# Kernel optimization log

Hardware: AMD Instinct MI355X
Metric: run time of the kernel (lower is better)

Reference implementation:

```python
import jax, jax.numpy as jnp
import numpy as np

B = 1024; PAST = 64; FUT = 16; N = PAST + FUT; DM = N // 3; HID = 64
EMB = [(2000, 32), (7, 8), (24, 8)]
OUTP = 3 + 32 + 8 + 8  # 51 = out_preprocess
O = OUTP - 1           # 50
HID1 = 64; HID2 = 64
NEG = -1e30  # finite stand-in for -inf so fully-masked rows stay NaN-free


def _gcnn(x, A, W, act):
    # D = diag((1 + rowsum(sign(relu(A-1e-15))))^-0.5); out = act(D @ A @ D @ (x W^T))
    d = (1.0 + (A > 1e-15).astype(x.dtype).sum(1)) ** -0.5
    An = d[:, None] * A * d[None, :]            # (P,P)
    h = jnp.einsum('pq,bqc->bpc', An, x @ W.T)  # (B,P,out)
    return jax.nn.relu(h) if act else h


def _forward(data, emb0, emb1, emb2, w1, b1, w2, b2, w3, b3,
             M, Wg1a, Wg1b, Wk, smoothing, Wg2a, Wg2b):
    # learned adjacency: masked softmax over strictly-lower-triangular support
    mask = jnp.tril(jnp.ones((N, N), data.dtype), -1)
    A0 = jax.nn.relu(M @ M.T)
    A = jax.nn.softmax(jnp.where(mask > 0, A0, NEG), axis=1)
    A = jnp.where(mask > 0, A, 0.0)
    # pre_processing: embeddings + MLP, then re-append last raw column
    tabs = (emb0, emb1, emb2)
    e = [t[data[:, :, i].astype(jnp.int32)] for i, t in enumerate(tabs)]
    h = jnp.concatenate(e + [data[:, :, -3:]], -1)        # (B,N,51)
    h = jax.nn.relu(h @ w1.T + b1)
    h = jax.nn.relu(h @ w2.T + b2)
    h = h @ w3.T + b3                                      # (B,N,50)
    x = jnp.concatenate([h, data[:, :, -1:]], -1)          # (B,N,51)
    sg1, sg2 = x[:, :PAST], x[:, PAST:]
    A11 = A[:PAST, :PAST]
    x1 = _gcnn(_gcnn(sg1, A11, Wg1a, True), A11, Wg1b, False)   # (B,PAST,50)
    xk = jnp.concatenate([x1, sg2[:, :, :-1]], 1)               # (B,N,50)
    y = x[:, :PAST, -1:]                                        # (B,PAST,1)
    # Kernel: batched Mahalanobis quadratic form (diagonal computed directly)
    xp, xf = xk[:, :PAST], xk[:, PAST:]
    theta = Wk @ Wk.T
    theta = (theta + theta.T) / 2
    diff = xp[:, None, :, :] - xf[:, :, None, :]                # (B,F,P,50)
    q = jnp.einsum('bjip,pq,bjiq->bji', diff, theta, diff)      # (B,F,P)
    alpha = -0.5 * q / (jax.nn.sigmoid(smoothing[0]) * 0.01)
    At = A[FUT:, :PAST] if False else A[PAST:, :PAST]           # (F,P)
    At = jax.nn.softmax(jnp.where(At != 0, At, NEG), axis=1)
    # torch Softmax(dim=1) on (B,F,P) normalizes over the F axis
    alpha = jax.nn.softmax(jnp.where(At[None] >= 0.004, alpha, NEG), axis=1)
    yh = jnp.einsum('bjp,bpo->bjo', alpha, y)                   # (B,F,1)
    x2 = jnp.concatenate([sg2[:, :, :-1], yh], -1)              # (B,F,51)
    A22 = A[PAST:, PAST:]
    out = _gcnn(_gcnn(x2, A22, Wg2a, True), A22, Wg2b, False).reshape(-1, FUT)
    # cdist(x, x), p=2, with NaN-safe sqrt at zero distance
    xc = jnp.concatenate([sg1, x2], 1)                          # (B,N,51)
    sq = jnp.sum(xc * xc, -1)
    d2 = jnp.maximum(sq[:, :, None] + sq[:, None, :]
                     - 2.0 * jnp.einsum('bnc,bmc->bnm', xc, xc), 0.0)
    dist = jnp.where(d2 > 0, jnp.sqrt(jnp.where(d2 > 0, d2, 1.0)), 0.0)
    return (out, dist, A)


def setup_inputs() -> dict:
    key = jax.random.key(0)
    ks = jax.random.split(key, 20)
    cols = [jax.random.randint(ks[i], (B, N, 1), 0, EMB[i][0]).astype(jnp.float32)
            for i in range(3)]
    data = jnp.concatenate(cols + [jax.random.normal(ks[3], (B, N, 3), jnp.float32)], -1)
    g = lambda k, s, sc: jax.random.normal(k, s, jnp.float32) * sc
    return dict(
        data=data,
        emb0=g(ks[4], EMB[0], 1.0),
        emb1=g(ks[5], EMB[1], 1.0),
        emb2=g(ks[6], EMB[2], 1.0),
        w1=g(ks[7], (128, OUTP), OUTP ** -0.5), b1=jnp.zeros((128,), jnp.float32),
        w2=g(ks[8], (128, 128), 128 ** -0.5), b2=jnp.zeros((128,), jnp.float32),
        w3=g(ks[9], (O, 128), 128 ** -0.5), b3=jnp.zeros((O,), jnp.float32),
        M=g(ks[10], (N, DM), 1.0),
        Wg1a=g(ks[11], (HID1, OUTP), OUTP ** -0.5),
        Wg1b=g(ks[12], (O, HID1), HID1 ** -0.5),
        Wk=g(ks[13], (O, HID), 0.05),
        smoothing=g(ks[14], (1,), 1.0),
        Wg2a=g(ks[15], (HID2, OUTP), OUTP ** -0.5),
        Wg2b=g(ks[16], (1, HID2), HID2 ** -0.5),
    )


def reference(data, emb0, emb1, emb2, w1, b1, w2, b2, w3, b3,
              M, Wg1a, Wg1b, Wk, smoothing, Wg2a, Wg2b):
    return _forward(data, emb0, emb1, emb2, w1, b1, w2, b2, w3, b3,
                    M, Wg1a, Wg1b, Wk, smoothing, Wg2a, Wg2b)
```

## Files before the change

kernel.cpp:

```cpp
#include <hip/hip_runtime.h>
#include <math.h>


#define NEGBIG (-1e30f)

#define OFF_X     0
#define OFF_A     7471104
#define OFF_AN22  7481600
#define OFF_MK    7484356
#define OFF_GAH   7514692
#define OFF_GAL   7516740
#define OFF_G2AT  7521156
#define OFF_SC    7524420
#define OFF_W1H   7524424
#define OFF_W1L   7528520
#define OFF_W2H   7532616
#define OFF_W2L   7540808
#define OFF_W3H   7549000
#define OFF_W3L   7553096
#define OFF_ANH   7557192
#define OFF_ANL   7559240
#define OFF_GBH   7561288
#define OFF_GBL   7563336
#define OFF_WKH   7565384
#define OFF_WKL   7567432

#define OUT_OUT   0
#define OUT_DIST  16384
#define OUT_A     6569984

typedef __attribute__((ext_vector_type(8))) short bf16x8;
typedef __attribute__((ext_vector_type(4))) short s16x4;
typedef __attribute__((ext_vector_type(4))) float f32x4;

__device__ __forceinline__ unsigned short f2bf(float x) {
  union { float f; unsigned u; } v; v.f = x;
  unsigned r = v.u + 0x7fffu + ((v.u >> 16) & 1u);
  return (unsigned short)(r >> 16);
}
__device__ __forceinline__ float bf2f(unsigned short h) {
  union { unsigned u; float f; } v; v.u = ((unsigned)h) << 16; return v.f;
}
__device__ __forceinline__ void split2(float v, unsigned short& h, unsigned short& l) {
  unsigned short hh = f2bf(v);
  h = hh;
  l = f2bf(v - bf2f(hh));
}
#define SWZ6(r, k) (((r) << 6) + (((((k) >> 3) ^ ((r) & 7)) << 3) | ((k) & 7)))
#define SWZ7(r, k) (((r) << 7) + (((((k) >> 3) ^ ((r) & 7)) << 3) | ((k) & 7)))

#define MFMA3(acc, aH, aL, bH, bL) \
  acc = __builtin_amdgcn_mfma_f32_16x16x32_bf16(aH, bH, acc, 0, 0, 0); \
  acc = __builtin_amdgcn_mfma_f32_16x16x32_bf16(aH, bL, acc, 0, 0, 0); \
  acc = __builtin_amdgcn_mfma_f32_16x16x32_bf16(aL, bH, acc, 0, 0, 0);
#define MFMA4(acc, aH, aL, bH, bL) \
  MFMA3(acc, aH, aL, bH, bL) \
  acc = __builtin_amdgcn_mfma_f32_16x16x32_bf16(aL, bL, acc, 0, 0, 0);

__global__ __launch_bounds__(256) void k_prep(
    const float* __restrict__ M, const float* __restrict__ Wk,
    const float* __restrict__ sm,
    const float* __restrict__ w1, const float* __restrict__ w2,
    const float* __restrict__ w3,
    const float* __restrict__ wg1a, const float* __restrict__ wg1b,
    const float* __restrict__ wg2a,
    float* __restrict__ ws, float* __restrict__ out)
{
  __shared__ float Msh[80 * 26];
  __shared__ float Ash[80 * 80];
  __shared__ float d1[64];
  __shared__ float d2s[16];
  const int t = threadIdx.x;

  if (blockIdx.x == 0) {
    for (int e = t; e < 80 * 26; e += 256) Msh[e] = M[e];
    __syncthreads();
    for (int e = t; e < 6400; e += 256) {
      int i = e / 80, j = e % 80;
      float v = 0.f;
      if (j < i) {
        float s = 0.f;
        for (int k = 0; k < 26; ++k) s += Msh[i * 26 + k] * Msh[j * 26 + k];
        v = s > 0.f ? s : 0.f;
      }
      Ash[e] = v;
    }
    __syncthreads();
    if (t > 0 && t < 80) {
      int i = t;
      float m = -3.4e38f;
      for (int j = 0; j < i; ++j) m = fmaxf(m, Ash[i * 80 + j]);
      float s = 0.f;
      for (int j = 0; j < i; ++j) {
        float e = expf(Ash[i * 80 + j] - m);
        Ash[i * 80 + j] = e;
        s += e;
      }
      float inv = 1.f / s;
      for (int j = 0; j < i; ++j) Ash[i * 80 + j] *= inv;
    }
    __syncthreads();
    {
      float* Aws = ws + OFF_A;
      float* Aout = out + OUT_A;
      for (int e = t; e < 6400; e += 256) { Aws[e] = Ash[e]; Aout[e] = Ash[e]; }
    }
    if (t < 64) {
      int c = 0;
      for (int j = 0; j < 64; ++j) if (Ash[t * 80 + j] > 1e-15f) ++c;
      d1[t] = 1.f / sqrtf(1.f + (float)c);
    } else if (t < 80) {
      int i = t - 64; int c = 0;
      for (int j = 0; j < 16; ++j) if (Ash[(64 + i) * 80 + 64 + j] > 1e-15f) ++c;
      d2s[i] = 1.f / sqrtf(1.f + (float)c);
    }
    __syncthreads();
    {
      float* an22 = ws + OFF_AN22;
      unsigned short* anH = (unsigned short*)(ws + OFF_ANH);
      unsigned short* anL = (unsigned short*)(ws + OFF_ANL);
      for (int e = t; e < 4096; e += 256) {
        int i = e >> 6, j = e & 63;
        float v = d1[i] * Ash[i * 80 + j] * d1[j];
        unsigned short h = f2bf(v);
        anH[e] = h; anL[e] = f2bf(v - bf2f(h));
      }
      for (int e = t; e < 256; e += 256) {
        int i = e >> 4, j = e & 15;
        an22[e] = d2s[i] * Ash[(64 + i) * 80 + 64 + j] * d2s[j];
      }
    }
    if (t < 16) {
      float* mk = ws + OFF_MK;
      int j = t;
      float m = -3.4e38f;
      for (int i = 0; i < 64; ++i) {
        float v = Ash[(64 + j) * 80 + i];
        v = (v != 0.f) ? v : NEGBIG;
        m = fmaxf(m, v);
      }
      float s = 0.f;
      for (int i = 0; i < 64; ++i) {
        float v = Ash[(64 + j) * 80 + i];
        v = (v != 0.f) ? v : NEGBIG;
        s += expf(v - m);
      }
      float inv = 1.f / s;
      for (int i = 0; i < 64; ++i) {
        float v = Ash[(64 + j) * 80 + i];
        v = (v != 0.f) ? v : NEGBIG;
        mk[j * 64 + i] = (expf(v - m) * inv >= 0.004f) ? 1.f : 0.f;
      }
    }
  } else if (blockIdx.x == 1) {
    unsigned short* wkh = (unsigned short*)(ws + OFF_WKH);
    unsigned short* wkl = (unsigned short*)(ws + OFF_WKL);
    for (int e = t; e < 4096; e += 256) {
      int h = e >> 6, o = e & 63;
      float v = (o < 50) ? Wk[o * 64 + h] : 0.f;
      unsigned short hh = f2bf(v);
      wkh[e] = hh; wkl[e] = f2bf(v - bf2f(hh));
    }
    if (t == 0) {
      float v = sm[0];
      float sig = 1.f / (1.f + expf(-v));
      (ws + OFF_SC)[0] = -0.5f / (sig * 0.01f);
    }
  } else if (blockIdx.x == 2) {
    unsigned short* w1h = (unsigned short*)(ws + OFF_W1H);
    unsigned short* w1l = (unsigned short*)(ws + OFF_W1L);
    for (int e = t; e < 8192; e += 256) {
      int n = e >> 6, k = e & 63;
      float v = (k < 51) ? w1[n * 51 + k] : 0.f;
      unsigned short h = f2bf(v);
      w1h[e] = h; w1l[e] = f2bf(v - bf2f(h));
    }
    unsigned short* w3h = (unsigned short*)(ws + OFF_W3H);
    unsigned short* w3l = (unsigned short*)(ws + OFF_W3L);
    for (int e = t; e < 8192; e += 256) {
      int n = e >> 7, k = e & 127;
      float v = (n < 50) ? w3[n * 128 + k] : 0.f;
      unsigned short h = f2bf(v);
      w3h[e] = h; w3l[e] = f2bf(v - bf2f(h));
    }
    unsigned short* gah = (unsigned short*)(ws + OFF_GAH);
    unsigned short* gal = (unsigned short*)(ws + OFF_GAL);
    for (int e = t; e < 4096; e += 256) {
      int n = e >> 6, k = e & 63;
      float v = (k < 51) ? wg1a[n * 51 + k] : 0.f;
      unsigned short h = f2bf(v);
      gah[e] = h; gal[e] = f2bf(v - bf2f(h));
    }
  } else {
    unsigned short* w2h = (unsigned short*)(ws + OFF_W2H);
    unsigned short* w2l = (unsigned short*)(ws + OFF_W2L);
    for (int e = t; e < 16384; e += 256) {
      int n = e >> 7, k = e & 127;
      float v = w2[n * 128 + k];
      unsigned short h = f2bf(v);
      w2h[e] = h; w2l[e] = f2bf(v - bf2f(h));
    }
    unsigned short* gbh = (unsigned short*)(ws + OFF_GBH);
    unsigned short* gbl = (unsigned short*)(ws + OFF_GBL);
    for (int e = t; e < 4096; e += 256) {
      int n = e >> 6, k = e & 63;
      float v = (n < 50) ? wg1b[n * 64 + k] : 0.f;
      unsigned short h = f2bf(v);
      gbh[e] = h; gbl[e] = f2bf(v - bf2f(h));
    }
    float* g2at = ws + OFF_G2AT;
    for (int e = t; e < 64 * 51; e += 256) { int o = e / 51, k = e % 51; g2at[k * 64 + o] = wg2a[e]; }
  }
}

__global__ __launch_bounds__(512) void k_mlp(
    const float* __restrict__ data,
    const float* __restrict__ emb0, const float* __restrict__ emb1,
    const float* __restrict__ emb2,
    const float* __restrict__ b1, const float* __restrict__ b2,
    const float* __restrict__ b3,
    float* __restrict__ ws)
{
  __shared__ __align__(16) unsigned short actH[64 * 128];
  __shared__ __align__(16) unsigned short actL[64 * 128];
  __shared__ __align__(16) unsigned short wbH[8192];
  __shared__ __align__(16) unsigned short wbL[8192];
  const int t = threadIdx.x;
  const int lane = t & 63, wave = t >> 6;
  const int s = wave & 3, half = wave >> 2;
  const int m16 = lane & 15, quad = lane >> 4;
  const int base = blockIdx.x * 64;
  const int row0 = s * 16;
  const int arow = row0 + m16;
  const unsigned short* w1h = (const unsigned short*)(ws + OFF_W1H);
  const unsigned short* w1l = (const unsigned short*)(ws + OFF_W1L);
  const unsigned short* w2h = (const unsigned short*)(ws + OFF_W2H);
  const unsigned short* w2l = (const unsigned short*)(ws + OFF_W2L);
  const unsigned short* w3h = (const unsigned short*)(ws + OFF_W3H);
  const unsigned short* w3l = (const unsigned short*)(ws + OFF_W3L);
  float* x = ws + OFF_X;

  for (int e = t; e < 4096; e += 512) {
    int r = e >> 6, c = e & 63;
    int g = base + r;
    float v = 0.f;
    if (c < 32)      { int i0 = (int)data[g * 6 + 0]; v = emb0[i0 * 32 + c]; }
    else if (c < 40) { int i1 = (int)data[g * 6 + 1]; v = emb1[i1 * 8 + (c - 32)]; }
    else if (c < 48) { int i2 = (int)data[g * 6 + 2]; v = emb2[i2 * 8 + (c - 40)]; }
    else if (c < 51) { v = data[g * 6 + 3 + (c - 48)]; }
    int idx = SWZ7(r, c);
    split2(v, actH[idx], actL[idx]);
  }
  for (int q = t; q < 1024; q += 512) {
    int col = q >> 3, c = q & 7;
    int dst = (col << 6) + ((c ^ (col & 7)) << 3);
    *(bf16x8*)(wbH + dst) = *(const bf16x8*)(w1h + (col << 6) + (c << 3));
    *(bf16x8*)(wbL + dst) = *(const bf16x8*)(w1l + (col << 6) + (c << 3));
  }
  bf16x8 pH[2], pL[2];
#pragma unroll
  for (int i = 0; i < 2; ++i) {
    int q = t + i * 512;
    int coll = q >> 4, c = q & 15;
    int src = (coll << 7) + (c << 3);
    pH[i] = *(const bf16x8*)(w2h + src);
    pL[i] = *(const bf16x8*)(w2l + src);
  }
  if (t < 64) x[(base + t) * 51 + 50] = data[(base + t) * 6 + 5];
  __syncthreads();

  {
    f32x4 acc[4];
#pragma unroll
    for (int n = 0; n < 4; ++n) acc[n] = (f32x4){0.f, 0.f, 0.f, 0.f};
#pragma unroll
    for (int kb8 = 0; kb8 < 8; kb8 += 4) {
      int ach = ((quad + kb8) ^ (m16 & 7)) << 3;
      bf16x8 aH = *(const bf16x8*)(actH + (arow << 7) + ach);
      bf16x8 aL = *(const bf16x8*)(actL + (arow << 7) + ach);
#pragma unroll
      for (int n = 0; n < 4; ++n) {
        const int col = (half * 4 + n) * 16 + m16;
        int boff = (col << 6) + ach;
        bf16x8 bH = *(const bf16x8*)(wbH + boff);
        bf16x8 bL = *(const bf16x8*)(wbL + boff);
        MFMA3(acc[n], aH, aL, bH, bL)
      }
    }
#pragma unroll
    for (int n = 0; n < 4; ++n) {
      const int col = (half * 4 + n) * 16 + m16;
      const float bias = b1[col];
#pragma unroll
      for (int r = 0; r < 4; ++r) {
        float v = acc[n][r] + bias; v = v > 0.f ? v : 0.f;
        int idx = SWZ7(row0 + quad * 4 + r, col);
        split2(v, actH[idx], actL[idx]);
      }
    }
  }
  __syncthreads();

#pragma unroll
  for (int i = 0; i < 2; ++i) {
    int q = t + i * 512;
    int coll = q >> 4, c = q & 15;
    int dst = (coll << 7) + ((c ^ (coll & 7)) << 3);
    *(bf16x8*)(wbH + dst) = pH[i];
    *(bf16x8*)(wbL + dst) = pL[i];
  }
#pragma unroll
  for (int i = 0; i < 2; ++i) {
    int q = t + i * 512;
    int coll = q >> 4, c = q & 15;
    int src = ((64 + coll) << 7) + (c << 3);
    pH[i] = *(const bf16x8*)(w2h + src);
    pL[i] = *(const bf16x8*)(w2l + src);
  }
  __syncthreads();

  f32x4 acc2[2][2];
#pragma unroll
  for (int a2 = 0; a2 < 2; ++a2)
#pragma unroll
    for (int n = 0; n < 2; ++n) acc2[a2][n] = (f32x4){0.f, 0.f, 0.f, 0.f};
#pragma unroll
  for (int kb8 = 0; kb8 < 16; kb8 += 4) {
    int ach = ((quad + kb8) ^ (m16 & 7)) << 3;
    bf16x8 aH = *(const bf16x8*)(actH + (arow << 7) + ach);
    bf16x8 aL = *(const bf16x8*)(actL + (arow << 7) + ach);
#pragma unroll
    for (int n = 0; n < 2; ++n) {
      const int cl = (half * 2 + n) * 16 + m16;
      int boff = (cl << 7) + ach;
      bf16x8 bH = *(const bf16x8*)(wbH + boff);
      bf16x8 bL = *(const bf16x8*)(wbL + boff);
      MFMA3(acc2[0][n], aH, aL, bH, bL)
    }
  }
  __syncthreads();

#pragma unroll
  for (int i = 0; i < 2; ++i) {
    int q = t + i * 512;
    int coll = q >> 4, c = q & 15;
    int dst = (coll << 7) + ((c ^ (coll & 7)) << 3);
    *(bf16x8*)(wbH + dst) = pH[i];
    *(bf16x8*)(wbL + dst) = pL[i];
  }
#pragma unroll
  for (int i = 0; i < 2; ++i) {
    int q = t + i * 512;
    int coll = q >> 4, c = q & 15;
    int src = (coll << 7) + (c << 3);
    pH[i] = *(const bf16x8*)(w3h + src);
    pL[i] = *(const bf16x8*)(w3l + src);
  }
  __syncthreads();

#pragma unroll
  for (int kb8 = 0; kb8 < 16; kb8 += 4) {
    int ach = ((quad + kb8) ^ (m16 & 7)) << 3;
    bf16x8 aH = *(const bf16x8*)(actH + (arow << 7) + ach);
    bf16x8 aL = *(const bf16x8*)(actL + (arow << 7) + ach);
#pragma unroll
    for (int n = 0; n < 2; ++n) {
      const int cl = (half * 2 + n) * 16 + m16;
      int boff = (cl << 7) + ach;
      bf16x8 bH = *(const bf16x8*)(wbH + boff);
      bf16x8 bL = *(const bf16x8*)(wbL + boff);
      MFMA3(acc2[1][n], aH, aL, bH, bL)
    }
  }
  __syncthreads();

#pragma unroll
  for (int hh = 0; hh < 2; ++hh) {
#pragma unroll
    for (int n = 0; n < 2; ++n) {
      const int col = hh * 64 + (half * 2 + n) * 16 + m16;
      const float bias = b2[col];
#pragma unroll
      for (int r = 0; r < 4; ++r) {
        float v = acc2[hh][n][r] + bias; v = v > 0.f ? v : 0.f;
        int idx = SWZ7(row0 + quad * 4 + r, col);
        split2(v, actH[idx], actL[idx]);
      }
    }
  }
#pragma unroll
  for (int i = 0; i < 2; ++i) {
    int q = t + i * 512;
    int coll = q >> 4, c = q & 15;
    int dst = (coll << 7) + ((c ^ (coll & 7)) << 3);
    *(bf16x8*)(wbH + dst) = pH[i];
    *(bf16x8*)(wbL + dst) = pL[i];
  }
  __syncthreads();

  {
    f32x4 acc[2];
#pragma unroll
    for (int n = 0; n < 2; ++n) acc[n] = (f32x4){0.f, 0.f, 0.f, 0.f};
#pragma unroll
    for (int kb8 = 0; kb8 < 16; kb8 += 4) {
      int ach = ((quad + kb8) ^ (m16 & 7)) << 3;
      bf16x8 aH = *(const bf16x8*)(actH + (arow << 7) + ach);
      bf16x8 aL = *(const bf16x8*)(actL + (arow << 7) + ach);
#pragma unroll
      for (int n = 0; n < 2; ++n) {
        const int col = (half * 2 + n) * 16 + m16;
        int boff = (col << 7) + ach;
        bf16x8 bH = *(const bf16x8*)(wbH + boff);
        bf16x8 bL = *(const bf16x8*)(wbL + boff);
        MFMA3(acc[n], aH, aL, bH, bL)
      }
    }
#pragma unroll
    for (int n = 0; n < 2; ++n) {
      const int col = (half * 2 + n) * 16 + m16;
      if (col < 50) {
        const float bias = b3[col];
#pragma unroll
        for (int r = 0; r < 4; ++r) {
          int row = row0 + quad * 4 + r;
          x[(base + row) * 51 + col] = acc[n][r] + bias;
        }
      }
    }
  }
}

__global__ __launch_bounds__(512) void k_gqd(const float* __restrict__ wg2b,
                                             float* __restrict__ ws,
                                             float* __restrict__ out)
{
  __shared__ __align__(16) unsigned short SH[32768];
  unsigned short* b1H = SH;
  unsigned short* b1L = SH + 4096;
  unsigned short* b2H = SH + 8192;
  unsigned short* b2L = SH + 12288;
  unsigned short* anH = SH + 16384;
  unsigned short* anL = SH + 20480;
  unsigned short* wH  = SH + 24576;
  unsigned short* wL  = SH + 28672;
  unsigned short* xfH = SH + 24576;
  unsigned short* xfL = SH + 25600;
  unsigned short* zfH = SH + 26624;
  unsigned short* zfL = SH + 27648;
  float* alS  = (float*)(SH + 28672);
  float* spH2 = (float*)(SH + 30848);
  float* spS  = (float*)(SH + 31104);
  float* sfS  = (float*)(SH + 31232);
  float* yvS  = (float*)(SH + 31264);
  float* yhsS = (float*)(SH + 31392);
  float* X2v  = (float*)(SH + 8192);
  float* A22v = X2v + 832;
  float* G2v  = A22v + 256;
  float* Pmv  = G2v + 1024;
  float* wb2  = Pmv + 1024;
  float* zzv  = wb2 + 64;
  unsigned short* xcH = SH;
  unsigned short* xcL = SH + 16384;
  float* sqS = (float*)(SH + 21504);

  const int t = threadIdx.x, b = blockIdx.x;
  const int lane = t & 63, wave = t >> 6;
  const int s = wave & 3, half = wave >> 2;
  const int m16 = lane & 15, quad = lane >> 4;
  const int row0 = s * 16;
  const int arow = row0 + m16;
  const float* x = ws + OFF_X;
  const float* mk = ws + OFF_MK;
  const float* an22 = ws + OFF_AN22;
  const float* g2at = ws + OFF_G2AT;
  const unsigned short* gAnH = (const unsigned short*)(ws + OFF_ANH);
  const unsigned short* gAnL = (const unsigned short*)(ws + OFF_ANL);
  const unsigned short* gaH = (const unsigned short*)(ws + OFF_GAH);
  const unsigned short* gaL = (const unsigned short*)(ws + OFF_GAL);
  const unsigned short* gbH = (const unsigned short*)(ws + OFF_GBH);
  const unsigned short* gbL = (const unsigned short*)(ws + OFF_GBL);
  const unsigned short* gwkH = (const unsigned short*)(ws + OFF_WKH);
  const unsigned short* gwkL = (const unsigned short*)(ws + OFF_WKL);
  const float sc = (ws + OFF_SC)[0];

  for (int e = t; e < 4096; e += 512) {
    int r = e >> 6, k = e & 63;
    float v = (k < 51) ? x[(b * 80 + r) * 51 + k] : 0.f;
    int idx = SWZ6(r, k);
    split2(v, b1H[idx], b1L[idx]);
  }
  {
    int q = t;
    if (q < 512) {
      int r = q >> 3, c = q & 7;
      int dst = (r << 6) + ((c ^ (r & 7)) << 3);
      int src = (r << 6) + (c << 3);
      *(bf16x8*)(anH + dst) = *(const bf16x8*)(gAnH + src);
      *(bf16x8*)(anL + dst) = *(const bf16x8*)(gAnL + src);
      *(bf16x8*)(wH + dst)  = *(const bf16x8*)(gaH + src);
      *(bf16x8*)(wL + dst)  = *(const bf16x8*)(gaL + src);
    }
  }
  float yvreg = 0.f;
  if (t < 64) yvreg = x[(b * 80 + t) * 51 + 50];
  bf16x8 pH, pL;
  {
    int q = t & 511;
    int r = q >> 3, c = q & 7;
    int src = (r << 6) + (c << 3);
    pH = *(const bf16x8*)(gbH + src);
    pL = *(const bf16x8*)(gbL + src);
  }
  __syncthreads();

  f32x4 accA[2];
#pragma unroll
  for (int n = 0; n < 2; ++n) accA[n] = (f32x4){0.f, 0.f, 0.f, 0.f};
#pragma unroll
  for (int kb8 = 0; kb8 < 8; kb8 += 4) {
    int ach = ((quad + kb8) ^ (m16 & 7)) << 3;
    bf16x8 aH = *(const bf16x8*)(b1H + (arow << 6) + ach);
    bf16x8 aL = *(const bf16x8*)(b1L + (arow << 6) + ach);
#pragma unroll
    for (int n = 0; n < 2; ++n) {
      const int col = (half * 2 + n) * 16 + m16;
      int boff = (col << 6) + ach;
      bf16x8 bH = *(const bf16x8*)(wH + boff);
      bf16x8 bL = *(const bf16x8*)(wL + boff);
      MFMA3(accA[n], aH, aL, bH, bL)
    }
  }
  __syncthreads();

  {
    const int kb = row0 + quad * 4;
#pragma unroll
    for (int n = 0; n < 2; ++n) {
      const int col = (half * 2 + n) * 16 + m16;
      int idx = (col << 6) + (((((kb >> 3) ^ (col & 7)) << 3)) | (kb & 7));
      s16x4 hv, lv;
#pragma unroll
      for (int r = 0; r < 4; ++r) {
        unsigned short hh, ll; split2(accA[n][r], hh, ll);
        hv[r] = (short)hh; lv[r] = (short)ll;
      }
      *(s16x4*)(b2H + idx) = hv; *(s16x4*)(b2L + idx) = lv;
    }
  }
  {
    int q = t & 511;
    int r = q >> 3, c = q & 7;
    int dst = (r << 6) + ((c ^ (r & 7)) << 3);
    *(bf16x8*)(wH + dst) = pH;
    *(bf16x8*)(wL + dst) = pL;
    int src = (r << 6) + (c << 3);
    pH = *(const bf16x8*)(gwkH + src);
    pL = *(const bf16x8*)(gwkL + src);
  }
  __syncthreads();

#pragma unroll
  for (int n = 0; n < 2; ++n) accA[n] = (f32x4){0.f, 0.f, 0.f, 0.f};
#pragma unroll
  for (int kb8 = 0; kb8 < 8; kb8 += 4) {
    int ach = ((quad + kb8) ^ (m16 & 7)) << 3;
    bf16x8 aH = *(const bf16x8*)(anH + (arow << 6) + ach);
    bf16x8 aL = *(const bf16x8*)(anL + (arow << 6) + ach);
#pragma unroll
    for (int n = 0; n < 2; ++n) {
      const int col = (half * 2 + n) * 16 + m16;
      int boff = (col << 6) + ach;
      bf16x8 bH = *(const bf16x8*)(b2H + boff);
      bf16x8 bL = *(const bf16x8*)(b2L + boff);
      MFMA3(accA[n], aH, aL, bH, bL)
    }
  }
  __syncthreads();

  {
    const int kb = row0 + quad * 4;
#pragma unroll
    for (int n = 0; n < 2; ++n) {
      const int col = (half * 2 + n) * 16 + m16;
      int idx = (col << 6) + (((((kb >> 3) ^ (col & 7)) << 3)) | (kb & 7));
      s16x4 hv, lv;
#pragma unroll
      for (int r = 0; r < 4; ++r) {
        float v = accA[n][r]; v = v > 0.f ? v : 0.f;
        unsigned short hh, ll; split2(v, hh, ll);
        hv[r] = (short)hh; lv[r] = (short)ll;
      }
      *(s16x4*)(b2H + idx) = hv; *(s16x4*)(b2L + idx) = lv;
    }
  }
  __syncthreads();

#pragma unroll
  for (int n = 0; n < 2; ++n) accA[n] = (f32x4){0.f, 0.f, 0.f, 0.f};
#pragma unroll
  for (int kb8 = 0; kb8 < 8; kb8 += 4) {
    int ach = ((quad + kb8) ^ (m16 & 7)) << 3;
    bf16x8 aH = *(const bf16x8*)(anH + (arow << 6) + ach);
    bf16x8 aL = *(const bf16x8*)(anL + (arow << 6) + ach);
#pragma unroll
    for (int n = 0; n < 2; ++n) {
      const int col = (half * 2 + n) * 16 + m16;
      int boff = (col << 6) + ach;
      bf16x8 bH = *(const bf16x8*)(b2H + boff);
      bf16x8 bL = *(const bf16x8*)(b2L + boff);
      MFMA3(accA[n], aH, aL, bH, bL)
    }
  }
  __syncthreads();

#pragma unroll
  for (int n = 0; n < 2; ++n) {
    const int col = (half * 2 + n) * 16 + m16;
#pragma unroll
    for (int r = 0; r < 4; ++r) {
      int idx = SWZ6(row0 + quad * 4 + r, col);
      split2(accA[n][r], b1H[idx], b1L[idx]);
    }
  }
  {
    int q = t & 511;
    int r = q >> 3, c = q & 7;
    int dst = (r << 6) + ((c ^ (r & 7)) << 3);
    *(bf16x8*)(anH + dst) = pH;
    *(bf16x8*)(anL + dst) = pL;
  }
  float xf0 = 0.f, xf1 = 0.f;
  {
    int e0 = t, e1 = t + 512;
    int r0r = e0 >> 6, c0 = e0 & 63;
    int r1r = e1 >> 6, c1 = e1 & 63;
    if (c0 < 50) xf0 = x[(b * 80 + 64 + r0r) * 51 + c0];
    if (c1 < 50) xf1 = x[(b * 80 + 64 + r1r) * 51 + c1];
  }
  __syncthreads();

#pragma unroll
  for (int n = 0; n < 2; ++n) accA[n] = (f32x4){0.f, 0.f, 0.f, 0.f};
#pragma unroll
  for (int kb8 = 0; kb8 < 8; kb8 += 4) {
    int ach = ((quad + kb8) ^ (m16 & 7)) << 3;
    bf16x8 aH = *(const bf16x8*)(b1H + (arow << 6) + ach);
    bf16x8 aL = *(const bf16x8*)(b1L + (arow << 6) + ach);
#pragma unroll
    for (int n = 0; n < 2; ++n) {
      const int col = (half * 2 + n) * 16 + m16;
      int boff = (col << 6) + ach;
      bf16x8 bH = *(const bf16x8*)(wH + boff);
      bf16x8 bL = *(const bf16x8*)(wL + boff);
      MFMA3(accA[n], aH, aL, bH, bL)
    }
  }
  __syncthreads();

#pragma unroll
  for (int n = 0; n < 2; ++n) {
    const int col = (half * 2 + n) * 16 + m16;
#pragma unroll
    for (int r = 0; r < 4; ++r) {
      int idx = SWZ6(row0 + quad * 4 + r, col);
      split2(accA[n][r], b2H[idx], b2L[idx]);
    }
  }
  {
    int e0 = t, e1 = t + 512;
    int i0 = SWZ6(e0 >> 6, e0 & 63);
    int i1 = SWZ6(e1 >> 6, e1 & 63);
    split2(xf0, xfH[i0], xfL[i0]);
    split2(xf1, xfH[i1], xfL[i1]);
  }
  if (t < 64) yvS[t] = yvreg;
  __syncthreads();

#pragma unroll
  for (int n = 0; n < 2; ++n) accA[n] = (f32x4){0.f, 0.f, 0.f, 0.f};
#pragma unroll
  for (int kb8 = 0; kb8 < 8; kb8 += 4) {
    int ach = ((quad + kb8) ^ (m16 & 7)) << 3;
    bf16x8 aH = *(const bf16x8*)(b2H + (arow << 6) + ach);
    bf16x8 aL = *(const bf16x8*)(b2L + (arow << 6) + ach);
#pragma unroll
    for (int n = 0; n < 2; ++n) {
      const int col = (half * 2 + n) * 16 + m16;
      int boff = (col << 6) + ach;
      bf16x8 bH = *(const bf16x8*)(anH + boff);
      bf16x8 bL = *(const bf16x8*)(anL + boff);
      MFMA4(accA[n], aH, aL, bH, bL)
    }
  }
  if (half == 0) {
    f32x4 af = (f32x4){0.f, 0.f, 0.f, 0.f};
#pragma unroll
    for (int kb8 = 0; kb8 < 8; kb8 += 4) {
      int ach = ((quad + kb8) ^ (m16 & 7)) << 3;
      bf16x8 aH = *(const bf16x8*)(xfH + (m16 << 6) + ach);
      bf16x8 aL = *(const bf16x8*)(xfL + (m16 << 6) + ach);
      const int col = s * 16 + m16;
      int boff = (col << 6) + ach;
      bf16x8 bH = *(const bf16x8*)(anH + boff);
      bf16x8 bL = *(const bf16x8*)(anL + boff);
      MFMA4(af, aH, aL, bH, bL)
    }
    const int h = s * 16 + m16;
#pragma unroll
    for (int r = 0; r < 4; ++r) {
      int idx = SWZ6(quad * 4 + r, h);
      split2(af[r], zfH[idx], zfL[idx]);
    }
  }
  {
    float s2[4];
#pragma unroll
    for (int r = 0; r < 4; ++r)
      s2[r] = accA[0][r] * accA[0][r] + accA[1][r] * accA[1][r];
#pragma unroll
    for (int n = 0; n < 2; ++n) {
      const int h = (half * 2 + n) * 16 + m16;
#pragma unroll
      for (int r = 0; r < 4; ++r) {
        int idx = SWZ6(row0 + quad * 4 + r, h);
        split2(accA[n][r], b1H[idx], b1L[idx]);
      }
    }
#pragma unroll
    for (int m = 1; m < 16; m <<= 1)
#pragma unroll
      for (int r = 0; r < 4; ++r) s2[r] += __shfl_xor(s2[r], m);
    if (m16 == 0) {
#pragma unroll
      for (int r = 0; r < 4; ++r)
        spH2[(row0 + quad * 4 + r) * 2 + half] = s2[r];
    }
  }
  __syncthreads();

  if (t < 64) {
    spS[t] = spH2[t * 2] + spH2[t * 2 + 1];
  } else if (t < 80) {
    int j = t - 64;
    float ssum = 0.f;
    for (int h = 0; h < 64; ++h) {
      int idx = SWZ6(j, h);
      float v = bf2f(zfH[idx]) + bf2f(zfL[idx]);
      ssum += v * v;
    }
    sfS[j] = ssum;
  }
  __syncthreads();

  {
    f32x4 ac2 = (f32x4){0.f, 0.f, 0.f, 0.f};
#pragma unroll
    for (int kb8 = 0; kb8 < 8; kb8 += 4) {
      int ach = ((quad + kb8) ^ (m16 & 7)) << 3;
      bf16x8 aH = *(const bf16x8*)(b1H + (arow << 6) + ach);
      bf16x8 aL = *(const bf16x8*)(b1L + (arow << 6) + ach);
      bf16x8 bH = *(const bf16x8*)(zfH + (m16 << 6) + ach);
      bf16x8 bL = *(const bf16x8*)(zfL + (m16 << 6) + ach);
      MFMA4(ac2, aH, aL, bH, bL)
    }
    if (half == 0) {
#pragma unroll
      for (int r = 0; r < 4; ++r) {
        int i = row0 + quad * 4 + r;
        alS[i * 17 + m16] = sc * (spS[i] + sfS[m16] - 2.f * ac2[r]);
      }
    }
  }
  __syncthreads();

  if (t < 64) {
    const int i = t;
    float lv[16];
    float m = -3.4e38f;
#pragma unroll
    for (int j = 0; j < 16; ++j) {
      float v = (mk[j * 64 + i] != 0.f) ? alS[i * 17 + j] : NEGBIG;
      lv[j] = v;
      m = fmaxf(m, v);
    }
    float ssum = 0.f;
#pragma unroll
    for (int j = 0; j < 16; ++j) { lv[j] = expf(lv[j] - m); ssum += lv[j]; }
    float inv = 1.f / ssum;
#pragma unroll
    for (int j = 0; j < 16; ++j) alS[i * 17 + j] = lv[j] * inv;
  }
  __syncthreads();

  if (t < 16) {
    float ssum = 0.f;
    for (int i = 0; i < 64; ++i) ssum += alS[i * 17 + t] * yvS[i];
    yhsS[t] = ssum;
  }
  __syncthreads();

  for (int e = t; e < 5120; e += 512) {
    int n = e >> 6, c = e & 63;
    float v = 0.f;
    if (c < 50)       v = x[(b * 80 + n) * 51 + c];
    else if (c == 50) v = (n < 64) ? x[(b * 80 + n) * 51 + 50] : yhsS[n - 64];
    int idx = SWZ6(n, c);
    split2(v, xcH[idx], xcL[idx]);
  }
  for (int e = t; e < 832; e += 512) {
    int r = e / 52, c = e - r * 52;
    float v = 0.f;
    if (c < 50)       v = x[(b * 80 + 64 + r) * 51 + c];
    else if (c == 50) v = yhsS[r];
    X2v[e] = v;
  }
  for (int e = t; e < 256; e += 512) A22v[e] = an22[e];
  if (t < 64) wb2[t] = wg2b[t];
  __syncthreads();

  f32x4 accD[4];
  {
    int tc = 0;
    for (int idx = wave; idx < 25; idx += 8) {
      int ts = idx / 5, tf = idx - ts * 5;
      f32x4 acc = (f32x4){0.f, 0.f, 0.f, 0.f};
#pragma unroll
      for (int kb8 = 0; kb8 < 8; kb8 += 4) {
        int ach = ((quad + kb8) ^ (m16 & 7)) << 3;
        bf16x8 aH = *(const bf16x8*)(xcH + ((ts * 16 + m16) << 6) + ach);
        bf16x8 aL = *(const bf16x8*)(xcL + ((ts * 16 + m16) << 6) + ach);
        const int col = tf * 16 + m16;
        int boff = (col << 6) + ach;
        bf16x8 bH = *(const bf16x8*)(xcH + boff);
        bf16x8 bL = *(const bf16x8*)(xcL + boff);
        MFMA3(acc, aH, aL, bH, bL)
      }
      if (ts == tf && (m16 >> 2) == quad) sqS[ts * 16 + m16] = acc[m16 & 3];
      accD[tc++] = acc;
    }
  }
  for (int e = t; e < 1024; e += 512) {
    int j = e >> 6, h = e & 63;
    float ssum = 0.f;
    for (int k = 0; k < 51; ++k) ssum += X2v[j * 52 + k] * g2at[k * 64 + h];
    G2v[e] = ssum;
  }
  __syncthreads();

  for (int e = t; e < 1024; e += 512) {
    int j = e >> 6, h = e & 63;
    float ssum = 0.f;
#pragma unroll
    for (int k = 0; k < 16; ++k) ssum += A22v[j * 16 + k] * G2v[k * 64 + h];
    Pmv[e] = ssum > 0.f ? ssum : 0.f;
  }
  {
    float* dist = out + OUT_DIST + b * 6400;
    int tc = 0;
    for (int idx = wave; idx < 25; idx += 8) {
      int ts = idx / 5, tf = idx - ts * 5;
      f32x4 acc = accD[tc++];
#pragma unroll
      for (int r = 0; r < 4; ++r) {
        int i = ts * 16 + quad * 4 + r;
        int m = tf * 16 + m16;
        float d2 = sqS[i] + sqS[m] - 2.f * acc[r];
        d2 = d2 > 0.f ? d2 : 0.f;
        dist[i * 80 + m] = d2 > 0.f ? sqrtf(d2) : 0.f;
      }
    }
  }
  __syncthreads();
  if (t < 16) {
    float ssum = 0.f;
    for (int h = 0; h < 64; ++h) ssum += Pmv[t * 64 + h] * wb2[h];
    zzv[t] = ssum;
  }
  __syncthreads();
  if (t < 16) {
    float ssum = 0.f;
#pragma unroll
    for (int k = 0; k < 16; ++k) ssum += A22v[t * 16 + k] * zzv[k];
    out[OUT_OUT + b * 16 + t] = ssum;
  }
}

extern "C" void kernel_launch(void* const* d_in, const int* in_sizes, int n_in,
                              void* d_out, int out_size, void* d_ws, size_t ws_size,
                              hipStream_t stream)
{
  const float* data = (const float*)d_in[0];
  const float* emb0 = (const float*)d_in[1];
  const float* emb1 = (const float*)d_in[2];
  const float* emb2 = (const float*)d_in[3];
  const float* w1   = (const float*)d_in[4];
  const float* b1   = (const float*)d_in[5];
  const float* w2   = (const float*)d_in[6];
  const float* b2   = (const float*)d_in[7];
  const float* w3   = (const float*)d_in[8];
  const float* b3   = (const float*)d_in[9];
  const float* M    = (const float*)d_in[10];
  const float* wg1a = (const float*)d_in[11];
  const float* wg1b = (const float*)d_in[12];
  const float* Wk   = (const float*)d_in[13];
  const float* smo  = (const float*)d_in[14];
  const float* wg2a = (const float*)d_in[15];
  const float* wg2b = (const float*)d_in[16];
  float* ws  = (float*)d_ws;
  float* out = (float*)d_out;

  k_prep<<<dim3(4),    dim3(256), 0, stream>>>(M, Wk, smo, w1, w2, w3, wg1a, wg1b, wg2a, ws, out);
  k_mlp <<<dim3(1280), dim3(512), 0, stream>>>(data, emb0, emb1, emb2, b1, b2, b3, ws);
  k_gqd <<<dim3(1024), dim3(512), 0, stream>>>(wg2b, ws, out);
}
```

Measured before the change: 212.2 us.

## Fuse preprocessing MLP into per-batch graph kernel and parallelize small reductions

Merges the MLP kernel into the per-batch GCN/kernel stage so each block computes its 80 rows of MLP output into shared memory instead of writing them to a global workspace and reading them back. Weights for the MLP are loaded directly from global memory into registers per wave rather than staged through LDS. Several serial 16-thread reductions are rewritten as 256-thread partial sums with shuffle reductions. The fusion removes a kernel launch and the global round trip for x, but adds about 16 KB of shared memory per block and a launch_bounds occupancy hint, which may affect occupancy.

```diff
diff --git a/kernel.cpp b/kernel.cpp
--- a/kernel.cpp
+++ b/kernel.cpp
@@ -213,229 +213,146 @@
   }
 }
 
-__global__ __launch_bounds__(512) void k_mlp(
+__global__ __launch_bounds__(512, 4) void k_fused(
     const float* __restrict__ data,
     const float* __restrict__ emb0, const float* __restrict__ emb1,
     const float* __restrict__ emb2,
-    const float* __restrict__ b1, const float* __restrict__ b2,
-    const float* __restrict__ b3,
-    float* __restrict__ ws)
-{
-  __shared__ __align__(16) unsigned short actH[64 * 128];
-  __shared__ __align__(16) unsigned short actL[64 * 128];
-  __shared__ __align__(16) unsigned short wbH[8192];
-  __shared__ __align__(16) unsigned short wbL[8192];
-  const int t = threadIdx.x;
-  const int lane = t & 63, wave = t >> 6;
-  const int s = wave & 3, half = wave >> 2;
-  const int m16 = lane & 15, quad = lane >> 4;
-  const int base = blockIdx.x * 64;
-  const int row0 = s * 16;
-  const int arow = row0 + m16;
-  const unsigned short* w1h = (const unsigned short*)(ws + OFF_W1H);
-  const unsigned short* w1l = (const unsigned short*)(ws + OFF_W1L);
-  const unsigned short* w2h = (const unsigned short*)(ws + OFF_W2H);
-  const unsigned short* w2l = (const unsigned short*)(ws + OFF_W2L);
-  const unsigned short* w3h = (const unsigned short*)(ws + OFF_W3H);
-  const unsigned short* w3l = (const unsigned short*)(ws + OFF_W3L);
-  float* x = ws + OFF_X;
-
-  for (int e = t; e < 4096; e += 512) {
-    int r = e >> 6, c = e & 63;
-    int g = base + r;
-    float v = 0.f;
-    if (c < 32)      { int i0 = (int)data[g * 6 + 0]; v = emb0[i0 * 32 + c]; }
-    else if (c < 40) { int i1 = (int)data[g * 6 + 1]; v = emb1[i1 * 8 + (c - 32)]; }
-    else if (c < 48) { int i2 = (int)data[g * 6 + 2]; v = emb2[i2 * 8 + (c - 40)]; }
-    else if (c < 51) { v = data[g * 6 + 3 + (c - 48)]; }
-    int idx = SWZ7(r, c);
-    split2(v, actH[idx], actL[idx]);
-  }
-  for (int q = t; q < 1024; q += 512) {
-    int col = q >> 3, c = q & 7;
-    int dst = (col << 6) + ((c ^ (col & 7)) << 3);
-    *(bf16x8*)(wbH + dst) = *(const bf16x8*)(w1h + (col << 6) + (c << 3));
-    *(bf16x8*)(wbL + dst) = *(const bf16x8*)(w1l + (col << 6) + (c << 3));
-  }
-  bf16x8 pH[2], pL[2];
-#pragma unroll
-  for (int i = 0; i < 2; ++i) {
-    int q = t + i * 512;
-    int coll = q >> 4, c = q & 15;
-    int src = (coll << 7) + (c << 3);
-    pH[i] = *(const bf16x8*)(w2h + src);
-    pL[i] = *(const bf16x8*)(w2l + src);
-  }
-  if (t < 64) x[(base + t) * 51 + 50] = data[(base + t) * 6 + 5];
-  __syncthreads();
-
-  {
-    f32x4 acc[4];
-#pragma unroll
-    for (int n = 0; n < 4; ++n) acc[n] = (f32x4){0.f, 0.f, 0.f, 0.f};
-#pragma unroll
-    for (int kb8 = 0; kb8 < 8; kb8 += 4) {
-      int ach = ((quad + kb8) ^ (m16 & 7)) << 3;
-      bf16x8 aH = *(const bf16x8*)(actH + (arow << 7) + ach);
-      bf16x8 aL = *(const bf16x8*)(actL + (arow << 7) + ach);
-#pragma unroll
-      for (int n = 0; n < 4; ++n) {
-        const int col = (half * 4 + n) * 16 + m16;
-        int boff = (col << 6) + ach;
-        bf16x8 bH = *(const bf16x8*)(wbH + boff);
-        bf16x8 bL = *(const bf16x8*)(wbL + boff);
-        MFMA3(acc[n], aH, aL, bH, bL)
-      }
-    }
-#pragma unroll
-    for (int n = 0; n < 4; ++n) {
-      const int col = (half * 4 + n) * 16 + m16;
-      const float bias = b1[col];
-#pragma unroll
-      for (int r = 0; r < 4; ++r) {
-        float v = acc[n][r] + bias; v = v > 0.f ? v : 0.f;
-        int idx = SWZ7(row0 + quad * 4 + r, col);
-        split2(v, actH[idx], actL[idx]);
-      }
-    }
-  }
-  __syncthreads();
-
-#pragma unroll
-  for (int i = 0; i < 2; ++i) {
-    int q = t + i * 512;
-    int coll = q >> 4, c = q & 15;
-    int dst = (coll << 7) + ((c ^ (coll & 7)) << 3);
-    *(bf16x8*)(wbH + dst) = pH[i];
-    *(bf16x8*)(wbL + dst) = pL[i];
-  }
-#pragma unroll
-  for (int i = 0; i < 2; ++i) {
-    int q = t + i * 512;
-    int coll = q >> 4, c = q & 15;
-    int src = ((64 + coll) << 7) + (c << 3);
-    pH[i] = *(const bf16x8*)(w2h + src);
-    pL[i] = *(const bf16x8*)(w2l + src);
-  }
-  __syncthreads();
-
-  f32x4 acc2[2][2];
-#pragma unroll
-  for (int a2 = 0; a2 < 2; ++a2)
-#pragma unroll
-    for (int n = 0; n < 2; ++n) acc2[a2][n] = (f32x4){0.f, 0.f, 0.f, 0.f};
-#pragma unroll
-  for (int kb8 = 0; kb8 < 16; kb8 += 4) {
-    int ach = ((quad + kb8) ^ (m16 & 7)) << 3;
-    bf16x8 aH = *(const bf16x8*)(actH + (arow << 7) + ach);
-    bf16x8 aL = *(const bf16x8*)(actL + (arow << 7) + ach);
-#pragma unroll
-    for (int n = 0; n < 2; ++n) {
-      const int cl = (half * 2 + n) * 16 + m16;
-      int boff = (cl << 7) + ach;
-      bf16x8 bH = *(const bf16x8*)(wbH + boff);
-      bf16x8 bL = *(const bf16x8*)(wbL + boff);
-      MFMA3(acc2[0][n], aH, aL, bH, bL)
-    }
-  }
-  __syncthreads();
-
-#pragma unroll
-  for (int i = 0; i < 2; ++i) {
-    int q = t + i * 512;
-    int coll = q >> 4, c = q & 15;
-    int dst = (coll << 7) + ((c ^ (coll & 7)) << 3);
-    *(bf16x8*)(wbH + dst) = pH[i];
-    *(bf16x8*)(wbL + dst) = pL[i];
-  }
-#pragma unroll
-  for (int i = 0; i < 2; ++i) {
-    int q = t + i * 512;
-    int coll = q >> 4, c = q & 15;
-    int src = (coll << 7) + (c << 3);
-    pH[i] = *(const bf16x8*)(w3h + src);
-    pL[i] = *(const bf16x8*)(w3l + src);
-  }
-  __syncthreads();
-
-#pragma unroll
-  for (int kb8 = 0; kb8 < 16; kb8 += 4) {
-    int ach = ((quad + kb8) ^ (m16 & 7)) << 3;
-    bf16x8 aH = *(const bf16x8*)(actH + (arow << 7) + ach);
-    bf16x8 aL = *(const bf16x8*)(actL + (arow << 7) + ach);
-#pragma unroll
-    for (int n = 0; n < 2; ++n) {
-      const int cl = (half * 2 + n) * 16 + m16;
-      int boff = (cl << 7) + ach;
-      bf16x8 bH = *(const bf16x8*)(wbH + boff);
-      bf16x8 bL = *(const bf16x8*)(wbL + boff);
-      MFMA3(acc2[1][n], aH, aL, bH, bL)
-    }
-  }
-  __syncthreads();
-
-#pragma unroll
-  for (int hh = 0; hh < 2; ++hh) {
-#pragma unroll
-    for (int n = 0; n < 2; ++n) {
-      const int col = hh * 64 + (half * 2 + n) * 16 + m16;
-      const float bias = b2[col];
-#pragma unroll
-      for (int r = 0; r < 4; ++r) {
-        float v = acc2[hh][n][r] + bias; v = v > 0.f ? v : 0.f;
-        int idx = SWZ7(row0 + quad * 4 + r, col);
-        split2(v, actH[idx], actL[idx]);
-      }
-    }
-  }
-#pragma unroll
-  for (int i = 0; i < 2; ++i) {
-    int q = t + i * 512;
-    int coll = q >> 4, c = q & 15;
-    int dst = (coll << 7) + ((c ^ (coll & 7)) << 3);
-    *(bf16x8*)(wbH + dst) = pH[i];
-    *(bf16x8*)(wbL + dst) = pL[i];
-  }
-  __syncthreads();
-
-  {
-    f32x4 acc[2];
-#pragma unroll
-    for (int n = 0; n < 2; ++n) acc[n] = (f32x4){0.f, 0.f, 0.f, 0.f};
-#pragma unroll
-    for (int kb8 = 0; kb8 < 16; kb8 += 4) {
-      int ach = ((quad + kb8) ^ (m16 & 7)) << 3;
-      bf16x8 aH = *(const bf16x8*)(actH + (arow << 7) + ach);
-      bf16x8 aL = *(const bf16x8*)(actL + (arow << 7) + ach);
-#pragma unroll
-      for (int n = 0; n < 2; ++n) {
-        const int col = (half * 2 + n) * 16 + m16;
-        int boff = (col << 7) + ach;
-        bf16x8 bH = *(const bf16x8*)(wbH + boff);
-        bf16x8 bL = *(const bf16x8*)(wbL + boff);
-        MFMA3(acc[n], aH, aL, bH, bL)
-      }
-    }
-#pragma unroll
-    for (int n = 0; n < 2; ++n) {
-      const int col = (half * 2 + n) * 16 + m16;
-      if (col < 50) {
-        const float bias = b3[col];
-#pragma unroll
-        for (int r = 0; r < 4; ++r) {
-          int row = row0 + quad * 4 + r;
-          x[(base + row) * 51 + col] = acc[n][r] + bias;
-        }
-      }
-    }
-  }
-}
-
-__global__ __launch_bounds__(512) void k_gqd(const float* __restrict__ wg2b,
-                                             float* __restrict__ ws,
-                                             float* __restrict__ out)
+    const float* __restrict__ b1v, const float* __restrict__ b2v,
+    const float* __restrict__ b3v,
+    const float* __restrict__ wg2b,
+    float* __restrict__ ws, float* __restrict__ out)
 {
   __shared__ __align__(16) unsigned short SH[32768];
+  __shared__ __align__(16) float xbuf[80 * 51];
+
+  const int t = threadIdx.x, b = blockIdx.x;
+  const int lane = t & 63, wave = t >> 6;
+  const int m16 = lane & 15, quad = lane >> 4;
+
+  {
+    unsigned short* mIaH = SH;
+    unsigned short* mIaL = SH + 5120;
+    unsigned short* mHdH = SH + 10240;
+    unsigned short* mHdL = SH + 20480;
+    const unsigned short* w1h = (const unsigned short*)(ws + OFF_W1H);
+    const unsigned short* w1l = (const unsigned short*)(ws + OFF_W1L);
+    const unsigned short* w2h = (const unsigned short*)(ws + OFF_W2H);
+    const unsigned short* w2l = (const unsigned short*)(ws + OFF_W2L);
+    const unsigned short* w3h = (const unsigned short*)(ws + OFF_W3H);
+    const unsigned short* w3l = (const unsigned short*)(ws + OFF_W3L);
+
+    for (int e = t; e < 5120; e += 512) {
+      int r = e >> 6, c = e & 63;
+      int g = b * 80 + r;
+      float v = 0.f;
+      if (c < 32)      { int i0 = (int)data[g * 6 + 0]; v = emb0[i0 * 32 + c]; }
+      else if (c < 40) { int i1 = (int)data[g * 6 + 1]; v = emb1[i1 * 8 + (c - 32)]; }
+      else if (c < 48) { int i2 = (int)data[g * 6 + 2]; v = emb2[i2 * 8 + (c - 40)]; }
+      else if (c < 51) { v = data[g * 6 + 3 + (c - 48)]; }
+      int idx = SWZ6(r, c);
+      split2(v, mIaH[idx], mIaL[idx]);
+    }
+    if (t < 80) xbuf[t * 51 + 50] = data[(b * 80 + t) * 6 + 5];
+    __syncthreads();
+
+    {
+      const int col = wave * 16 + m16;
+      bf16x8 bH0 = *(const bf16x8*)(w1h + (col << 6) + (quad << 3));
+      bf16x8 bL0 = *(const bf16x8*)(w1l + (col << 6) + (quad << 3));
+      bf16x8 bH1 = *(const bf16x8*)(w1h + (col << 6) + ((quad + 4) << 3));
+      bf16x8 bL1 = *(const bf16x8*)(w1l + (col << 6) + ((quad + 4) << 3));
+      const float bias = b1v[col];
+      const int ach0 = ((quad + 0) ^ (m16 & 7)) << 3;
+      const int ach1 = ((quad + 4) ^ (m16 & 7)) << 3;
+#pragma unroll
+      for (int rt = 0; rt < 5; ++rt) {
+        const int ar = rt * 16 + m16;
+        f32x4 acc = (f32x4){0.f, 0.f, 0.f, 0.f};
+        bf16x8 aH = *(const bf16x8*)(mIaH + (ar << 6) + ach0);
+        bf16x8 aL = *(const bf16x8*)(mIaL + (ar << 6) + ach0);
+        MFMA3(acc, aH, aL, bH0, bL0)
+        aH = *(const bf16x8*)(mIaH + (ar << 6) + ach1);
+        aL = *(const bf16x8*)(mIaL + (ar << 6) + ach1);
+        MFMA3(acc, aH, aL, bH1, bL1)
+#pragma unroll
+        for (int r = 0; r < 4; ++r) {
+          float v = acc[r] + bias; v = v > 0.f ? v : 0.f;
+          int idx = SWZ7(rt * 16 + quad * 4 + r, col);
+          split2(v, mHdH[idx], mHdL[idx]);
+        }
+      }
+    }
+    __syncthreads();
+
+    f32x4 acc2[5];
+    {
+      const int col = wave * 16 + m16;
+      bf16x8 bh[4], bl[4];
+#pragma unroll
+      for (int kk = 0; kk < 4; ++kk) {
+        bh[kk] = *(const bf16x8*)(w2h + (col << 7) + ((quad + kk * 4) << 3));
+        bl[kk] = *(const bf16x8*)(w2l + (col << 7) + ((quad + kk * 4) << 3));
+      }
+#pragma unroll
+      for (int rt = 0; rt < 5; ++rt) {
+        const int ar = rt * 16 + m16;
+        f32x4 acc = (f32x4){0.f, 0.f, 0.f, 0.f};
+#pragma unroll
+        for (int kk = 0; kk < 4; ++kk) {
+          int ach = ((quad + kk * 4) ^ (m16 & 7)) << 3;
+          bf16x8 aH = *(const bf16x8*)(mHdH + (ar << 7) + ach);
+          bf16x8 aL = *(const bf16x8*)(mHdL + (ar << 7) + ach);
+          MFMA3(acc, aH, aL, bh[kk], bl[kk])
+        }
+        acc2[rt] = acc;
+      }
+    }
+    __syncthreads();
+    {
+      const int col = wave * 16 + m16;
+      const float bias = b2v[col];
+#pragma unroll
+      for (int rt = 0; rt < 5; ++rt) {
+#pragma unroll
+        for (int r = 0; r < 4; ++r) {
+          float v = acc2[rt][r] + bias; v = v > 0.f ? v : 0.f;
+          int idx = SWZ7(rt * 16 + quad * 4 + r, col);
+          split2(v, mHdH[idx], mHdL[idx]);
+        }
+      }
+    }
+    __syncthreads();
+
+    {
+      const int ct = wave & 3, rh = wave >> 2;
+      const int col = ct * 16 + m16;
+      bf16x8 bh[4], bl[4];
+#pragma unroll
+      for (int kk = 0; kk < 4; ++kk) {
+        bh[kk] = *(const bf16x8*)(w3h + (col << 7) + ((quad + kk * 4) << 3));
+        bl[kk] = *(const bf16x8*)(w3l + (col << 7) + ((quad + kk * 4) << 3));
+      }
+      const float bias = (col < 50) ? b3v[col] : 0.f;
+      for (int rt = rh; rt < 5; rt += 2) {
+        const int ar = rt * 16 + m16;
+        f32x4 acc = (f32x4){0.f, 0.f, 0.f, 0.f};
+#pragma unroll
+        for (int kk = 0; kk < 4; ++kk) {
+          int ach = ((quad + kk * 4) ^ (m16 & 7)) << 3;
+          bf16x8 aH = *(const bf16x8*)(mHdH + (ar << 7) + ach);
+          bf16x8 aL = *(const bf16x8*)(mHdL + (ar << 7) + ach);
+          MFMA3(acc, aH, aL, bh[kk], bl[kk])
+        }
+        if (col < 50) {
+#pragma unroll
+          for (int r = 0; r < 4; ++r)
+            xbuf[(rt * 16 + quad * 4 + r) * 51 + col] = acc[r] + bias;
+        }
+      }
+    }
+    __syncthreads();
+  }
+
   unsigned short* b1H = SH;
   unsigned short* b1L = SH + 4096;
   unsigned short* b2H = SH + 8192;
@@ -464,13 +381,9 @@
   unsigned short* xcL = SH + 16384;
   float* sqS = (float*)(SH + 21504);
 
-  const int t = threadIdx.x, b = blockIdx.x;
-  const int lane = t & 63, wave = t >> 6;
   const int s = wave & 3, half = wave >> 2;
-  const int m16 = lane & 15, quad = lane >> 4;
   const int row0 = s * 16;
   const int arow = row0 + m16;
-  const float* x = ws + OFF_X;
   const float* mk = ws + OFF_MK;
   const float* an22 = ws + OFF_AN22;
   const float* g2at = ws + OFF_G2AT;
@@ -486,7 +399,7 @@
 
   for (int e = t; e < 4096; e += 512) {
     int r = e >> 6, k = e & 63;
-    float v = (k < 51) ? x[(b * 80 + r) * 51 + k] : 0.f;
+    float v = (k < 51) ? xbuf[r * 51 + k] : 0.f;
     int idx = SWZ6(r, k);
     split2(v, b1H[idx], b1L[idx]);
   }
@@ -503,7 +416,7 @@
     }
   }
   float yvreg = 0.f;
-  if (t < 64) yvreg = x[(b * 80 + t) * 51 + 50];
+  if (t < 64) yvreg = xbuf[t * 51 + 50];
   bf16x8 pH, pL;
   {
     int q = t & 511;
@@ -635,8 +548,8 @@
     int e0 = t, e1 = t + 512;
     int r0r = e0 >> 6, c0 = e0 & 63;
     int r1r = e1 >> 6, c1 = e1 & 63;
-    if (c0 < 50) xf0 = x[(b * 80 + 64 + r0r) * 51 + c0];
-    if (c1 < 50) xf1 = x[(b * 80 + 64 + r1r) * 51 + c1];
+    if (c0 < 50) xf0 = xbuf[(64 + r0r) * 51 + c0];
+    if (c1 < 50) xf1 = xbuf[(64 + r1r) * 51 + c1];
   }
   __syncthreads();
 
@@ -741,15 +654,19 @@
 
   if (t < 64) {
     spS[t] = spH2[t * 2] + spH2[t * 2 + 1];
-  } else if (t < 80) {
-    int j = t - 64;
-    float ssum = 0.f;
-    for (int h = 0; h < 64; ++h) {
-      int idx = SWZ6(j, h);
-      float v = bf2f(zfH[idx]) + bf2f(zfL[idx]);
-      ssum += v * v;
-    }
-    sfS[j] = ssum;
+  } else if (t < 320) {
+    int idx = t - 64;
+    int j = idx >> 4, h0 = (idx & 15) * 4;
+    float p = 0.f;
+#pragma unroll
+    for (int r = 0; r < 4; ++r) {
+      int ii = SWZ6(j, h0 + r);
+      float v = bf2f(zfH[ii]) + bf2f(zfL[ii]);
+      p += v * v;
+    }
+#pragma unroll
+    for (int m = 1; m < 16; m <<= 1) p += __shfl_xor(p, m);
+    if ((idx & 15) == 0) sfS[j] = p;
   }
   __syncthreads();
 
@@ -793,25 +710,29 @@
   }
   __syncthreads();
 
-  if (t < 16) {
-    float ssum = 0.f;
-    for (int i = 0; i < 64; ++i) ssum += alS[i * 17 + t] * yvS[i];
-    yhsS[t] = ssum;
+  if (t < 256) {
+    int j = t >> 4, i0 = (t & 15) * 4;
+    float p = 0.f;
+#pragma unroll
+    for (int r = 0; r < 4; ++r) p += alS[(i0 + r) * 17 + j] * yvS[i0 + r];
+#pragma unroll
+    for (int m = 1; m < 16; m <<= 1) p += __shfl_xor(p, m);
+    if ((t & 15) == 0) yhsS[j] = p;
   }
   __syncthreads();
 
   for (int e = t; e < 5120; e += 512) {
     int n = e >> 6, c = e & 63;
     float v = 0.f;
-    if (c < 50)       v = x[(b * 80 + n) * 51 + c];
-    else if (c == 50) v = (n < 64) ? x[(b * 80 + n) * 51 + 50] : yhsS[n - 64];
+    if (c < 50)       v = xbuf[n * 51 + c];
+    else if (c == 50) v = (n < 64) ? xbuf[n * 51 + 50] : yhsS[n - 64];
     int idx = SWZ6(n, c);
     split2(v, xcH[idx], xcL[idx]);
   }
   for (int e = t; e < 832; e += 512) {
     int r = e / 52, c = e - r * 52;
     float v = 0.f;
-    if (c < 50)       v = x[(b * 80 + 64 + r) * 51 + c];
+    if (c < 50)       v = xbuf[(64 + r) * 51 + c];
     else if (c == 50) v = yhsS[r];
     X2v[e] = v;
   }
@@ -872,10 +793,14 @@
     }
   }
   __syncthreads();
-  if (t < 16) {
-    float ssum = 0.f;
-    for (int h = 0; h < 64; ++h) ssum += Pmv[t * 64 + h] * wb2[h];
-    zzv[t] = ssum;
+  if (t < 256) {
+    int j = t >> 4, h0 = (t & 15) * 4;
+    float p = 0.f;
+#pragma unroll
+    for (int r = 0; r < 4; ++r) p += Pmv[j * 64 + h0 + r] * wb2[h0 + r];
+#pragma unroll
+    for (int m = 1; m < 16; m <<= 1) p += __shfl_xor(p, m);
+    if ((t & 15) == 0) zzv[j] = p;
   }
   __syncthreads();
   if (t < 16) {
@@ -910,7 +835,6 @@
   float* ws  = (float*)d_ws;
   float* out = (float*)d_out;
 
-  k_prep<<<dim3(4),    dim3(256), 0, stream>>>(M, Wk, smo, w1, w2, w3, wg1a, wg1b, wg2a, ws, out);
-  k_mlp <<<dim3(1280), dim3(512), 0, stream>>>(data, emb0, emb1, emb2, b1, b2, b3, ws);
-  k_gqd <<<dim3(1024), dim3(512), 0, stream>>>(wg2b, ws, out);
+  k_prep <<<dim3(4),    dim3(256), 0, stream>>>(M, Wk, smo, w1, w2, w3, wg1a, wg1b, wg2a, ws, out);
+  k_fused<<<dim3(1024), dim3(512), 0, stream>>>(data, emb0, emb1, emb2, b1, b2, b3, wg2b, ws, out);
 }
```

After: 200.3 us. 5.6% less time.
